# Kernel tuning notes

Measured on AMD Instinct MI355X. Metric: run time of the kernel, lower is better.

Reference implementation:

```python
import jax, jax.numpy as jnp
import numpy as np
import math

EMBED_DIM = 1024
HEAD_DIM = 64
BATCH = 4
SEQ = 4096


def setup_inputs() -> dict:
    key = jax.random.key(0)
    k1, k2 = jax.random.split(key)
    x = jax.random.normal(k1, (BATCH, SEQ, EMBED_DIM), dtype=jnp.float32)
    QKV = jax.random.normal(k2, (EMBED_DIM, 3 * HEAD_DIM), dtype=jnp.float32) * (1.0 / math.sqrt(EMBED_DIM))
    return {"x": x, "QKV": QKV}


def reference(x, QKV):
    head_dim = QKV.shape[-1] // 3
    scale = 1.0 / math.sqrt(head_dim)
    qkv = x @ QKV                      # [b, s, 3*d]
    q, k, v = jnp.split(qkv, 3, axis=-1)
    scores = jnp.einsum('bqd,bkd->bqk', q, k) * scale  # [b, s, s]
    weights = jax.nn.softmax(scores, axis=-1)
    out = jnp.einsum('bqk,bkd->bqd', weights, v)        # [b, s, d]
    return out
```

## Files before the change

### kernel.cpp

```cpp
#include <hip/hip_runtime.h>
#include <hip/hip_bf16.h>

#define BATCH 4
#define SEQ   4096
#define EMB   1024
#define HD    64
#define N3    192
#define NSPLIT 8

typedef __attribute__((ext_vector_type(8)))  short short8;
typedef __attribute__((ext_vector_type(4)))  float floatx4;
typedef __attribute__((ext_vector_type(16))) float floatx16;
typedef unsigned long long ull;
typedef unsigned short us;

#define SSCALE 0.1803368801111204f

static __device__ __forceinline__ us f2bf(float f) {
    unsigned int u = __float_as_uint(f);
    u += 0x7fffu + ((u >> 16) & 1u);
    return (us)(u >> 16);
}
static __device__ __forceinline__ float bf2f(us h) {
    return __uint_as_float((unsigned int)h << 16);
}
static __device__ __forceinline__ unsigned int cvtpk(float lo, float hi) {
    unsigned int r;
    asm("v_cvt_pk_bf16_f32 %0, %1, %2" : "=v"(r) : "v"(lo), "v"(hi));
    return r;
}
static __device__ __forceinline__ void gll16(const void* g, void* l) {
    __builtin_amdgcn_global_load_lds(
        (const __attribute__((address_space(1))) unsigned int*)(unsigned long long)g,
        (__attribute__((address_space(3))) unsigned int*)(unsigned int)(unsigned long long)l,
        16, 0, 0);
}

#define MFMA16(A, B, C) __builtin_amdgcn_mfma_f32_16x16x32_bf16(A, B, C, 0, 0, 0)
#define MFMA32(A, B, C) __builtin_amdgcn_mfma_f32_32x32x16_bf16(A, B, C, 0, 0, 0)

__global__ __launch_bounds__(256) void wt_prep(const float* __restrict__ w,
                                               us* __restrict__ wf)
{
    int t = blockIdx.x * 256 + threadIdx.x;
    int l  = t & 63;
    int cb = (t >> 6) % 12;
    int kb = t / (64 * 12);
    int kbase = kb * 32 + (l >> 4) * 8;
    int n = cb * 16 + (l & 15);
    us e[8];
#pragma unroll
    for (int i = 0; i < 8; ++i)
        e[i] = f2bf(w[(size_t)(kbase + i) * N3 + n]);
    *(short8*)(wf + (size_t)t * 8) = *(short8*)e;
}

__global__ __launch_bounds__(512, 2) void qkv_proj(
    const float* __restrict__ x, const us* __restrict__ wf,
    us* __restrict__ q, us* __restrict__ k, us* __restrict__ vt)
{
    const int tid = threadIdx.x;
    const int w   = tid >> 6;
    const int l   = tid & 63;
    const int ln  = l & 15;
    const int g   = l >> 4;
    const int wm  = w >> 2;
    const int wn  = w & 3;
    const int row0 = blockIdx.x * 32;

    __shared__ __align__(16) char Xs[2][16384];

    const int srow  = tid >> 5;
    const int sunit = tid & 31;

    auto stage = [&](int c) {
#pragma unroll
        for (int i = 0; i < 2; ++i) {
            int row = i * 16 + srow;
            gll16(x + (size_t)(row0 + row) * EMB + c * 128 + ((sunit ^ (row & 7)) << 2),
                  Xs[c & 1] + i * 8192 + tid * 16);
        }
    };

    stage(0);

    floatx4 acc[3];
#pragma unroll
    for (int ng = 0; ng < 3; ++ng) acc[ng] = (floatx4){0.f, 0.f, 0.f, 0.f};

    const int rowl = wm * 16 + ln;

    for (int c = 0; c < 8; ++c) {
        asm volatile("s_waitcnt vmcnt(0)" ::: "memory");
        __builtin_amdgcn_sched_barrier(0);
        __syncthreads();

        short8 wfr[4][3];
#pragma unroll
        for (int ks = 0; ks < 4; ++ks)
#pragma unroll
            for (int ng = 0; ng < 3; ++ng)
                wfr[ks][ng] = *(const short8*)(wf +
                    ((size_t)((c * 4 + ks) * 12 + wn * 3 + ng) * 64 + l) * 8);
        asm volatile("" ::: "memory");

        if (c < 7) stage(c + 1);

        const char* Bx = Xs[c & 1];
#pragma unroll
        for (int ks = 0; ks < 4; ++ks) {
            int ub = ks * 8 + g * 2;
            float4 a0 = *(const float4*)(Bx + rowl * 512 + (((ub + 0) ^ (rowl & 7)) << 4));
            float4 a1 = *(const float4*)(Bx + rowl * 512 + (((ub + 1) ^ (rowl & 7)) << 4));
            unsigned int p0 = cvtpk(a0.x, a0.y), p1 = cvtpk(a0.z, a0.w);
            unsigned int p2 = cvtpk(a1.x, a1.y), p3 = cvtpk(a1.z, a1.w);
            int4 av = {(int)p0, (int)p1, (int)p2, (int)p3};
            short8 af = *(short8*)&av;
#pragma unroll
            for (int ng = 0; ng < 3; ++ng)
                acc[ng] = MFMA16(af, wfr[ks][ng], acc[ng]);
        }
    }

#pragma unroll
    for (int ng = 0; ng < 3; ++ng) {
        int n = wn * 48 + ng * 16 + ln;
#pragma unroll
        for (int j = 0; j < 4; ++j) {
            int grow = row0 + wm * 16 + g * 4 + j;
            int b = grow >> 12;
            int s = grow & 4095;
            if (n < 64)
                q[(size_t)(b * SEQ + s) * HD + n] = f2bf(acc[ng][j] * SSCALE);
            else if (n < 128)
                k[(size_t)(b * SEQ + s) * HD + (n - 64)] = f2bf(acc[ng][j]);
            else
                vt[((size_t)b * HD + (n - 128)) * SEQ + s] = f2bf(acc[ng][j]);
        }
    }
}

__global__ __launch_bounds__(256, 4) void attn(
    const us* __restrict__ qg, const us* __restrict__ kg,
    const us* __restrict__ vtg, us* __restrict__ pob, float* __restrict__ pml)
{
    const int tid = threadIdx.x;
    const int w   = tid >> 6;
    const int l   = tid & 63;
    const int qn  = l & 31;
    const int u   = l >> 5;
    const int bid = blockIdx.x;
    const int split = bid & 7;
    const int qt  = (bid >> 3) & 31;
    const int b   = bid >> 8;
    const int qr0 = qt * 128 + w * 32;

    __shared__ __align__(16) char LDSbuf[32768];

    const us* kbase = kg  + (size_t)b * SEQ * HD;
    const us* vbase = vtg + (size_t)b * HD * SEQ;

    const us* qrow = qg + ((size_t)(b * SEQ) + qr0 + qn) * HD;
    short8 qf[4];
#pragma unroll
    for (int t = 0; t < 4; ++t) qf[t] = *(const short8*)(qrow + t * 16 + u * 8);

    const int ktbase = split * 8;

    auto stage = [&](int ktg, char* Kd, char* Vd) {
#pragma unroll
        for (int j = 0; j < 2; ++j) {
            int idx = w * 2 + j;
            int row = idx * 8 + (l >> 3);
            int c16 = (l & 7) ^ (row & 7);
            gll16(kbase + (size_t)(ktg * 64 + row) * HD + c16 * 8, Kd + idx * 1024);
            gll16(vbase + (size_t)row * SEQ + ktg * 64 + c16 * 8, Vd + idx * 1024);
        }
    };

    stage(ktbase, LDSbuf, LDSbuf + 8192);

    floatx16 o0 = {}, o1 = {};
    float m_run = -1e30f, l_run = 0.f;

    for (int kt = 0; kt < 8; ++kt) {
        asm volatile("s_waitcnt vmcnt(0)" ::: "memory");
        __syncthreads();
        char* Ks = LDSbuf + (kt & 1) * 16384;
        char* Vs = Ks + 8192;
        if (kt < 7) {
            char* Kn = LDSbuf + ((kt + 1) & 1) * 16384;
            stage(ktbase + kt + 1, Kn, Kn + 8192);
        }

        floatx16 sa0 = {}, sa1 = {};
        __builtin_amdgcn_s_setprio(1);
#pragma unroll
        for (int t = 0; t < 4; ++t) {
            int r0 = qn, r1 = 32 + qn;
            short8 kf0 = *(const short8*)(Ks + r0 * 128 + ((32 * t + 16 * u) ^ ((r0 & 7) << 4)));
            short8 kf1 = *(const short8*)(Ks + r1 * 128 + ((32 * t + 16 * u) ^ ((r1 & 7) << 4)));
            sa0 = MFMA32(kf0, qf[t], sa0);
            sa1 = MFMA32(kf1, qf[t], sa1);
        }
        __builtin_amdgcn_s_setprio(0);

        float tm = sa0[0];
#pragma unroll
        for (int r = 1; r < 16; ++r) tm = fmaxf(tm, sa0[r]);
#pragma unroll
        for (int r = 0; r < 16; ++r) tm = fmaxf(tm, sa1[r]);
        tm = fmaxf(tm, __shfl_xor(tm, 32));

        if (!__all(tm <= m_run + 8.f)) {
            float mn  = fmaxf(m_run, tm);
            float fac = exp2f(m_run - mn);
            m_run = mn;
            l_run *= fac;
#pragma unroll
            for (int r = 0; r < 16; ++r) { o0[r] *= fac; o1[r] *= fac; }
        }
        float ls = 0.f;
#pragma unroll
        for (int r = 0; r < 16; ++r) { float p = exp2f(sa0[r] - m_run); sa0[r] = p; ls += p; }
#pragma unroll
        for (int r = 0; r < 16; ++r) { float p = exp2f(sa1[r] - m_run); sa1[r] = p; ls += p; }
        ls += __shfl_xor(ls, 32);
        l_run += ls;

        __builtin_amdgcn_s_setprio(1);
#pragma unroll
        for (int s = 0; s < 4; ++s) {
            unsigned int A0, A1, B0, B1;
            if (s == 0) {
                A0 = cvtpk(sa0[0], sa0[1]);  A1 = cvtpk(sa0[2], sa0[3]);
                B0 = cvtpk(sa0[4], sa0[5]);  B1 = cvtpk(sa0[6], sa0[7]);
            } else if (s == 1) {
                A0 = cvtpk(sa0[8], sa0[9]);  A1 = cvtpk(sa0[10], sa0[11]);
                B0 = cvtpk(sa0[12], sa0[13]); B1 = cvtpk(sa0[14], sa0[15]);
            } else if (s == 2) {
                A0 = cvtpk(sa1[0], sa1[1]);  A1 = cvtpk(sa1[2], sa1[3]);
                B0 = cvtpk(sa1[4], sa1[5]);  B1 = cvtpk(sa1[6], sa1[7]);
            } else {
                A0 = cvtpk(sa1[8], sa1[9]);  A1 = cvtpk(sa1[10], sa1[11]);
                B0 = cvtpk(sa1[12], sa1[13]); B1 = cvtpk(sa1[14], sa1[15]);
            }
            asm("v_permlane32_swap_b32 %0, %1" : "+v"(A0), "+v"(B0));
            asm("v_permlane32_swap_b32 %0, %1" : "+v"(A1), "+v"(B1));
            int4 pbv = {(int)A0, (int)A1, (int)B0, (int)B1};
            short8 pb = *(short8*)&pbv;

            int rv0 = qn, rv1 = 32 + qn;
            short8 vf0 = *(const short8*)(Vs + rv0 * 128 + ((32 * s + 16 * u) ^ ((rv0 & 7) << 4)));
            short8 vf1 = *(const short8*)(Vs + rv1 * 128 + ((32 * s + 16 * u) ^ ((rv1 & 7) << 4)));
            o0 = MFMA32(vf0, pb, o0);
            o1 = MFMA32(vf1, pb, o1);
        }
        __builtin_amdgcn_s_setprio(0);
    }

    __syncthreads();
    float* Ts = (float*)(LDSbuf + w * 8192);
#pragma unroll
    for (int r = 0; r < 16; ++r) {
        int d = (r & 3) + 8 * (r >> 2) + 4 * u;
        Ts[d * 32 + qn]        = o0[r];
        Ts[(d + 32) * 32 + qn] = o1[r];
    }
    __builtin_amdgcn_s_waitcnt(0);
    const size_t prow0 = (size_t)split * (BATCH * SEQ) + (size_t)b * SEQ + qr0;
#pragma unroll
    for (int c = 0; c < 8; ++c) {
        float v0 = Ts[(u * 32 + c * 4 + 0) * 32 + qn];
        float v1 = Ts[(u * 32 + c * 4 + 1) * 32 + qn];
        float v2 = Ts[(u * 32 + c * 4 + 2) * 32 + qn];
        float v3 = Ts[(u * 32 + c * 4 + 3) * 32 + qn];
        ull pk =  (ull)f2bf(v0) | ((ull)f2bf(v1) << 16)
               | ((ull)f2bf(v2) << 32) | ((ull)f2bf(v3) << 48);
        *(ull*)(pob + (prow0 + qn) * HD + u * 32 + c * 4) = pk;
    }
    if (l < 32) {
        pml[(prow0 + l) * 2 + 0] = m_run;
        pml[(prow0 + l) * 2 + 1] = l_run;
    }
}

__global__ __launch_bounds__(256) void recombine(
    const us* __restrict__ pob, const float* __restrict__ pml,
    float* __restrict__ out)
{
    int idx = blockIdx.x * 256 + threadIdx.x;
    int row = idx >> 3;
    int c8  = idx & 7;

    float m[NSPLIT], lv[NSPLIT];
#pragma unroll
    for (int i = 0; i < NSPLIT; ++i) {
        m[i]  = pml[((size_t)i * (BATCH * SEQ) + row) * 2 + 0];
        lv[i] = pml[((size_t)i * (BATCH * SEQ) + row) * 2 + 1];
    }
    float M = m[0];
#pragma unroll
    for (int i = 1; i < NSPLIT; ++i) M = fmaxf(M, m[i]);
    float wt[NSPLIT], denom = 0.f;
#pragma unroll
    for (int i = 0; i < NSPLIT; ++i) { wt[i] = exp2f(m[i] - M); denom += wt[i] * lv[i]; }
    float inv = 1.0f / denom;

    float acc[8];
#pragma unroll
    for (int e = 0; e < 8; ++e) acc[e] = 0.f;
#pragma unroll
    for (int i = 0; i < NSPLIT; ++i) {
        short8 v = *(const short8*)(pob + ((size_t)i * (BATCH * SEQ) + row) * HD + c8 * 8);
#pragma unroll
        for (int e = 0; e < 8; ++e) acc[e] += wt[i] * bf2f((us)v[e]);
    }
    float4 r0 = {acc[0] * inv, acc[1] * inv, acc[2] * inv, acc[3] * inv};
    float4 r1 = {acc[4] * inv, acc[5] * inv, acc[6] * inv, acc[7] * inv};
    *(float4*)(out + (size_t)row * HD + c8 * 8)     = r0;
    *(float4*)(out + (size_t)row * HD + c8 * 8 + 4) = r1;
}

extern "C" void kernel_launch(void* const* d_in, const int* in_sizes, int n_in,
                              void* d_out, int out_size, void* d_ws, size_t ws_size,
                              hipStream_t stream) {
    (void)in_sizes; (void)n_in; (void)out_size; (void)ws_size;
    const float* x = (const float*)d_in[0];
    const float* w = (const float*)d_in[1];
    float* out = (float*)d_out;

    const size_t QE = (size_t)BATCH * SEQ * HD;
    us* q   = (us*)d_ws;
    us* k   = q + QE;
    us* vt  = k + QE;
    us* wfb = vt + QE;
    us* pob = wfb + (size_t)N3 * EMB;
    float* pml = (float*)(pob + (size_t)NSPLIT * BATCH * SEQ * HD);

    wt_prep  <<<dim3(96),   dim3(256), 0, stream>>>(w, wfb);
    qkv_proj <<<dim3(512),  dim3(512), 0, stream>>>(x, wfb, q, k, vt);
    attn     <<<dim3(1024), dim3(256), 0, stream>>>(q, k, vt, pob, pml);
    recombine<<<dim3(512),  dim3(256), 0, stream>>>(pob, pml, out);
}
```

Before: 151.8 us.

## Double block sizes in QKV projection and attention, tree-reduce softmax max/sum

Makes the QKV projection and attention blocks twice as large: each attention block now covers 256 query rows with 8 waves sharing one K/V tile stage, and each projection block covers 64 rows. The intent is to halve per-block K/V and weight staging traffic and raise reuse of LDS tiles. The softmax row max and row sum switch from serial chains to tree reductions to shorten dependency chains. The output transpose now runs in two serialized rounds through shared memory, which adds barriers. The projection kernel's launch bounds of (1024,4) may force register pressure or spilling.

```diff
diff --git a/kernel.cpp b/kernel.cpp
--- a/kernel.cpp
+++ b/kernel.cpp
@@ -55,7 +55,7 @@
     *(short8*)(wf + (size_t)t * 8) = *(short8*)e;
 }
 
-__global__ __launch_bounds__(512, 2) void qkv_proj(
+__global__ __launch_bounds__(1024, 4) void qkv_proj(
     const float* __restrict__ x, const us* __restrict__ wf,
     us* __restrict__ q, us* __restrict__ k, us* __restrict__ vt)
 {
@@ -66,19 +66,18 @@
     const int g   = l >> 4;
     const int wm  = w >> 2;
     const int wn  = w & 3;
-    const int row0 = blockIdx.x * 32;
-
-    __shared__ __align__(16) char Xs[2][16384];
-
-    const int srow  = tid >> 5;
-    const int sunit = tid & 31;
+    const int row0 = blockIdx.x * 64;
+
+    __shared__ __align__(16) char Xs[2][32768];
 
     auto stage = [&](int c) {
 #pragma unroll
         for (int i = 0; i < 2; ++i) {
-            int row = i * 16 + srow;
-            gll16(x + (size_t)(row0 + row) * EMB + c * 128 + ((sunit ^ (row & 7)) << 2),
-                  Xs[c & 1] + i * 8192 + tid * 16);
+            int unit = i * 1024 + tid;
+            int row  = unit >> 5;
+            int su   = unit & 31;
+            gll16(x + (size_t)(row0 + row) * EMB + c * 128 + ((su ^ (row & 7)) << 2),
+                  Xs[c & 1] + unit * 16);
         }
     };
 
@@ -140,7 +139,7 @@
     }
 }
 
-__global__ __launch_bounds__(256, 4) void attn(
+__global__ __launch_bounds__(512, 4) void attn(
     const us* __restrict__ qg, const us* __restrict__ kg,
     const us* __restrict__ vtg, us* __restrict__ pob, float* __restrict__ pml)
 {
@@ -151,9 +150,9 @@
     const int u   = l >> 5;
     const int bid = blockIdx.x;
     const int split = bid & 7;
-    const int qt  = (bid >> 3) & 31;
-    const int b   = bid >> 8;
-    const int qr0 = qt * 128 + w * 32;
+    const int qt  = (bid >> 3) & 15;
+    const int b   = bid >> 7;
+    const int qr0 = qt * 256 + w * 32;
 
     __shared__ __align__(16) char LDSbuf[32768];
 
@@ -168,14 +167,10 @@
     const int ktbase = split * 8;
 
     auto stage = [&](int ktg, char* Kd, char* Vd) {
-#pragma unroll
-        for (int j = 0; j < 2; ++j) {
-            int idx = w * 2 + j;
-            int row = idx * 8 + (l >> 3);
-            int c16 = (l & 7) ^ (row & 7);
-            gll16(kbase + (size_t)(ktg * 64 + row) * HD + c16 * 8, Kd + idx * 1024);
-            gll16(vbase + (size_t)row * SEQ + ktg * 64 + c16 * 8, Vd + idx * 1024);
-        }
+        int row = tid >> 3;
+        int c16 = (tid & 7) ^ (row & 7);
+        gll16(kbase + (size_t)(ktg * 64 + row) * HD + c16 * 8, Kd + tid * 16);
+        gll16(vbase + (size_t)row * SEQ + ktg * 64 + c16 * 8, Vd + tid * 16);
     };
 
     stage(ktbase, LDSbuf, LDSbuf + 8192);
@@ -205,12 +200,14 @@
         }
         __builtin_amdgcn_s_setprio(0);
 
-        float tm = sa0[0];
-#pragma unroll
-        for (int r = 1; r < 16; ++r) tm = fmaxf(tm, sa0[r]);
-#pragma unroll
-        for (int r = 0; r < 16; ++r) tm = fmaxf(tm, sa1[r]);
-        tm = fmaxf(tm, __shfl_xor(tm, 32));
+        float red[16];
+#pragma unroll
+        for (int r = 0; r < 16; ++r) red[r] = fmaxf(sa0[r], sa1[r]);
+#pragma unroll
+        for (int s = 8; s > 0; s >>= 1)
+#pragma unroll
+            for (int r = 0; r < s; ++r) red[r] = fmaxf(red[r], red[r + s]);
+        float tm = fmaxf(red[0], __shfl_xor(red[0], 32));
 
         if (!__all(tm <= m_run + 8.f)) {
             float mn  = fmaxf(m_run, tm);
@@ -220,13 +217,18 @@
 #pragma unroll
             for (int r = 0; r < 16; ++r) { o0[r] *= fac; o1[r] *= fac; }
         }
-        float ls = 0.f;
-#pragma unroll
-        for (int r = 0; r < 16; ++r) { float p = exp2f(sa0[r] - m_run); sa0[r] = p; ls += p; }
-#pragma unroll
-        for (int r = 0; r < 16; ++r) { float p = exp2f(sa1[r] - m_run); sa1[r] = p; ls += p; }
-        ls += __shfl_xor(ls, 32);
-        l_run += ls;
+#pragma unroll
+        for (int r = 0; r < 16; ++r) { sa0[r] = exp2f(sa0[r] - m_run); }
+#pragma unroll
+        for (int r = 0; r < 16; ++r) { sa1[r] = exp2f(sa1[r] - m_run); }
+        float sred[16];
+#pragma unroll
+        for (int r = 0; r < 16; ++r) sred[r] = sa0[r] + sa1[r];
+#pragma unroll
+        for (int s = 8; s > 0; s >>= 1)
+#pragma unroll
+            for (int r = 0; r < s; ++r) sred[r] += sred[r + s];
+        l_run += sred[0] + __shfl_xor(sred[0], 32);
 
         __builtin_amdgcn_s_setprio(1);
 #pragma unroll
@@ -259,25 +261,29 @@
         __builtin_amdgcn_s_setprio(0);
     }
 
-    __syncthreads();
-    float* Ts = (float*)(LDSbuf + w * 8192);
-#pragma unroll
-    for (int r = 0; r < 16; ++r) {
-        int d = (r & 3) + 8 * (r >> 2) + 4 * u;
-        Ts[d * 32 + qn]        = o0[r];
-        Ts[(d + 32) * 32 + qn] = o1[r];
-    }
-    __builtin_amdgcn_s_waitcnt(0);
     const size_t prow0 = (size_t)split * (BATCH * SEQ) + (size_t)b * SEQ + qr0;
-#pragma unroll
-    for (int c = 0; c < 8; ++c) {
-        float v0 = Ts[(u * 32 + c * 4 + 0) * 32 + qn];
-        float v1 = Ts[(u * 32 + c * 4 + 1) * 32 + qn];
-        float v2 = Ts[(u * 32 + c * 4 + 2) * 32 + qn];
-        float v3 = Ts[(u * 32 + c * 4 + 3) * 32 + qn];
-        ull pk =  (ull)f2bf(v0) | ((ull)f2bf(v1) << 16)
-               | ((ull)f2bf(v2) << 32) | ((ull)f2bf(v3) << 48);
-        *(ull*)(pob + (prow0 + qn) * HD + u * 32 + c * 4) = pk;
+    float* Ts = (float*)(LDSbuf + (w & 3) * 8192);
+#pragma unroll
+    for (int round = 0; round < 2; ++round) {
+        __syncthreads();
+        if ((w >> 2) == round) {
+#pragma unroll
+            for (int r = 0; r < 16; ++r) {
+                int d = (r & 3) + 8 * (r >> 2) + 4 * u;
+                Ts[d * 32 + qn]        = o0[r];
+                Ts[(d + 32) * 32 + qn] = o1[r];
+            }
+#pragma unroll
+            for (int c = 0; c < 8; ++c) {
+                float v0 = Ts[(u * 32 + c * 4 + 0) * 32 + qn];
+                float v1 = Ts[(u * 32 + c * 4 + 1) * 32 + qn];
+                float v2 = Ts[(u * 32 + c * 4 + 2) * 32 + qn];
+                float v3 = Ts[(u * 32 + c * 4 + 3) * 32 + qn];
+                ull pk =  (ull)f2bf(v0) | ((ull)f2bf(v1) << 16)
+                       | ((ull)f2bf(v2) << 32) | ((ull)f2bf(v3) << 48);
+                *(ull*)(pob + (prow0 + qn) * HD + u * 32 + c * 4) = pk;
+            }
+        }
     }
     if (l < 32) {
         pml[(prow0 + l) * 2 + 0] = m_run;
@@ -338,8 +344,8 @@
     us* pob = wfb + (size_t)N3 * EMB;
     float* pml = (float*)(pob + (size_t)NSPLIT * BATCH * SEQ * HD);
 
-    wt_prep  <<<dim3(96),   dim3(256), 0, stream>>>(w, wfb);
-    qkv_proj <<<dim3(512),  dim3(512), 0, stream>>>(x, wfb, q, k, vt);
-    attn     <<<dim3(1024), dim3(256), 0, stream>>>(q, k, vt, pob, pml);
-    recombine<<<dim3(512),  dim3(256), 0, stream>>>(pob, pml, out);
-}
+    wt_prep  <<<dim3(96),   dim3(256),  0, stream>>>(w, wfb);
+    qkv_proj <<<dim3(256),  dim3(1024), 0, stream>>>(x, wfb, q, k, vt);
+    attn     <<<dim3(512),  dim3(512),  0, stream>>>(q, k, vt, pob, pml);
+    recombine<<<dim3(512),  dim3(256),  0, stream>>>(pob, pml, out);
+}
```

Result: slower. 157.7 us (+3.9%).
